# Kernel tuning notes

Measured on AMD Instinct MI355X. Metric: run time of the kernel, lower is better.

## Reference

```python
import jax, jax.numpy as jnp
import numpy as np

B, NV, NRINGS, NDIRS, NF = 4, 50000, 3, 16, 16


def setup_inputs() -> dict:
    key = jax.random.key(0)
    k1, k2, k3, k4 = jax.random.split(key, 4)
    basepoints = jax.random.normal(k1, (B, NV, 3), dtype=jnp.float32)
    local_frames = jax.random.normal(k2, (B, NV, 3, 3), dtype=jnp.float32)
    # expmap: gather_nd indices into basepoints' (batch, vertex) dims
    vidx = jax.random.randint(k3, (B, NV, NRINGS, NDIRS), 0, NV, dtype=jnp.int32)
    bidx = jnp.broadcast_to(jnp.arange(B, dtype=jnp.int32)[:, None, None, None],
                            (B, NV, NRINGS, NDIRS))
    expmap = jnp.stack([bidx, vidx], axis=-1)  # (B, NV, NRINGS, NDIRS, 2)
    kernel = jax.random.normal(k4, (NRINGS, NDIRS, 3, NF), dtype=jnp.float32) * 0.05
    bias = jnp.zeros((NF,), dtype=jnp.float32)
    return {"basepoints": basepoints, "local_frames": local_frames,
            "expmap": expmap, "kernel": kernel, "bias": bias}


def reference(basepoints, local_frames, expmap, kernel, bias):
    b, nv = basepoints.shape[0], basepoints.shape[1]
    nrings, ndirs = expmap.shape[2], expmap.shape[3]
    nf = kernel.shape[-1]
    # gather_nd: neighbor coordinates per (ring, direction)
    y = basepoints[expmap[..., 0], expmap[..., 1]]          # (b, nv, nrings, ndirs, 3)
    # center at basepoint
    y = y - basepoints[:, :, None, None, :]
    # rotate into local frame
    y = jnp.einsum('bvkl,bvrdl->bvrdk', local_frames, y)    # (b, nv, nrings, ndirs, 3)
    # patch conv with ring wraparound (circular padding along direction axis)
    y = y.reshape(b * nv, nrings, ndirs, 3)
    y = jnp.concatenate([y, y[:, :, :-1, :]], axis=2)       # (b*nv, nrings, 2*ndirs-1, 3)
    y = jax.lax.conv_general_dilated(
        y, kernel, window_strides=(1, 1), padding='VALID',
        dimension_numbers=('NHWC', 'HWIO', 'NHWC'))         # (b*nv, 1, ndirs, nf)
    y = y.reshape(b, nv, ndirs, nf) + bias
    return jax.nn.relu(y)
```

## Files before the change

kernel.cpp:

```cpp
#include <hip/hip_runtime.h>

#define NBATCH 4
#define NV     50000
#define NRINGS 3
#define NDIRS  16
#define NF     16
#define VPB    16
#define YLS    148
#define KTS    20

__global__ __launch_bounds__(256, 4)
void input3d_kernel(const float* __restrict__ bp,
                    const float* __restrict__ fr,
                    const int2*  __restrict__ em,
                    const float* __restrict__ kw,
                    const float* __restrict__ bias,
                    float*       __restrict__ out)
{
    __shared__ __align__(16) float kt[NRINGS * 3 * NF * KTS];
    __shared__ __align__(16) float yl[VPB * YLS];
    __shared__ __align__(16) float ost[VPB * NDIRS * NF];

    const int tid = threadIdx.x;
    const int bv0 = blockIdx.x * VPB;

    for (int i = tid; i < NRINGS * NDIRS * 3 * NF; i += 256) {
        int f  = i & 15;
        int c  = (i >> 4) % 3;
        int dd = (i / 48) & 15;
        int r  = i / 768;
        kt[((r * 3 + c) * 16 + f) * KTS + dd] = kw[i];
    }

    #pragma unroll
    for (int k = 0; k < 3; ++k) {
        int p   = tid + k * 256;
        int v   = p / 48;
        int i48 = p - v * 48;
        int bv  = bv0 + v;
        int2 e  = em[bv * 48 + i48];
        int nb  = e.x * NV + e.y;
        float cx = bp[bv * 3 + 0];
        float cy = bp[bv * 3 + 1];
        float cz = bp[bv * 3 + 2];
        float d0 = bp[nb * 3 + 0] - cx;
        float d1 = bp[nb * 3 + 1] - cy;
        float d2 = bp[nb * 3 + 2] - cz;
        const float* F = fr + (size_t)bv * 9;
        #pragma unroll
        for (int c = 0; c < 3; ++c) {
            float yv = F[c * 3 + 0] * d0
                     + F[c * 3 + 1] * d1
                     + F[c * 3 + 2] * d2;
            yl[v * YLS + c * 48 + i48] = yv;
        }
    }
    __syncthreads();

    const int vloc = tid >> 4;
    const int f    = tid & 15;
    float acc[16];
    #pragma unroll
    for (int d = 0; d < 16; ++d) acc[d] = 0.f;

    const float* ylv = &yl[vloc * YLS];
    #pragma unroll 1
    for (int rc = 0; rc < 9; ++rc) {
        int r = rc / 3;
        int c = rc - r * 3;
        float ylr[16];
        const float4* y4 = (const float4*)(ylv + c * 48 + r * 16);
        *(float4*)&ylr[0]  = y4[0];
        *(float4*)&ylr[4]  = y4[1];
        *(float4*)&ylr[8]  = y4[2];
        *(float4*)&ylr[12] = y4[3];
        float kf[16];
        const float4* k4 = (const float4*)&kt[(rc * 16 + f) * KTS];
        *(float4*)&kf[0]  = k4[0];
        *(float4*)&kf[4]  = k4[1];
        *(float4*)&kf[8]  = k4[2];
        *(float4*)&kf[12] = k4[3];
        #pragma unroll
        for (int dd = 0; dd < 16; ++dd) {
            float kv = kf[dd];
            #pragma unroll
            for (int d = 0; d < 16; ++d)
                acc[d] = fmaf(ylr[(d + dd) & 15], kv, acc[d]);
        }
    }

    float bsf = bias[f];
    #pragma unroll
    for (int d = 0; d < 16; ++d) {
        float o = acc[d] + bsf;
        ost[vloc * 256 + d * 16 + f] = o > 0.f ? o : 0.f;
    }
    __syncthreads();

    const float4* s4 = (const float4*)&ost[tid * 16];
    float4* dst = (float4*)(out + (size_t)bv0 * 256 + (size_t)tid * 16);
    dst[0] = s4[0];
    dst[1] = s4[1];
    dst[2] = s4[2];
    dst[3] = s4[3];
}

extern "C" void kernel_launch(void* const* d_in, const int* in_sizes, int n_in,
                              void* d_out, int out_size, void* d_ws, size_t ws_size,
                              hipStream_t stream) {
    const float* bp   = (const float*)d_in[0];
    const float* fr   = (const float*)d_in[1];
    const int2*  em   = (const int2*)d_in[2];
    const float* kw   = (const float*)d_in[3];
    const float* bias = (const float*)d_in[4];
    float* out = (float*)d_out;

    const int total_bv = NBATCH * NV;
    const int grid = total_bv / VPB;
    input3d_kernel<<<grid, 256, 0, stream>>>(bp, fr, em, kw, bias, out);
}
```

Before: 414.0 us.

## Recast circular patch conv as bf16 MFMA GEMM over duplicated ring buffer

Reformulates the per-vertex circular convolution as a 16x144x16 GEMM run on MFMA 16x16x32 bf16 instructions. Rotated neighbor coordinates are stored in bf16 into a doubled, shifted LDS layout so each output direction row reads a contiguous window. Kernel weights are converted to bf16 straight into registers per lane, and outputs are written directly from the accumulators without the LDS staging pass. The aim is to replace about 2300 scalar FMAs per thread with a few matrix ops, at the cost of reduced precision from bf16 inputs and less coalesced output stores.

```diff
diff --git a/kernel.cpp b/kernel.cpp
--- a/kernel.cpp
+++ b/kernel.cpp
@@ -1,108 +1,123 @@
 #include <hip/hip_runtime.h>
+#include <hip/hip_bf16.h>
 
 #define NBATCH 4
 #define NV     50000
-#define NRINGS 3
-#define NDIRS  16
-#define NF     16
 #define VPB    16
-#define YLS    148
-#define KTS    20
+#define VST    304
+
+typedef __attribute__((ext_vector_type(8))) short short8;
+typedef __attribute__((ext_vector_type(4))) float floatx4;
 
 __global__ __launch_bounds__(256, 4)
-void input3d_kernel(const float* __restrict__ bp,
-                    const float* __restrict__ fr,
-                    const int2*  __restrict__ em,
-                    const float* __restrict__ kw,
-                    const float* __restrict__ bias,
-                    float*       __restrict__ out)
+void input3d_mfma(const float* __restrict__ bp,
+                  const float* __restrict__ fr,
+                  const int2*  __restrict__ em,
+                  const float* __restrict__ kw,
+                  const float* __restrict__ bias,
+                  float*       __restrict__ out)
 {
-    __shared__ __align__(16) float kt[NRINGS * 3 * NF * KTS];
-    __shared__ __align__(16) float yl[VPB * YLS];
-    __shared__ __align__(16) float ost[VPB * NDIRS * NF];
+    __shared__ __align__(16) unsigned short yls[VPB * 2 * VST];
 
-    const int tid = threadIdx.x;
-    const int bv0 = blockIdx.x * VPB;
+    const int tid  = threadIdx.x;
+    const int bv0  = blockIdx.x * VPB;
+    const int lane = tid & 63;
+    const int wid  = tid >> 6;
+    const int fcol = lane & 15;
+    const int quad = lane >> 4;
 
-    for (int i = tid; i < NRINGS * NDIRS * 3 * NF; i += 256) {
-        int f  = i & 15;
-        int c  = (i >> 4) % 3;
-        int dd = (i / 48) & 15;
-        int r  = i / 768;
-        kt[((r * 3 + c) * 16 + f) * KTS + dd] = kw[i];
+    for (int i = tid; i < VPB * 51; i += 256) {
+        int v = i / 51;
+        int w = i - v * 51;
+        int off = (w < 25) ? (279 + w) : (VST + 278 + (w - 25));
+        yls[v * 2 * VST + off] = 0;
     }
 
+    union WU { short s[8]; short8 v; };
+    WU wf[5];
     #pragma unroll
-    for (int k = 0; k < 3; ++k) {
-        int p   = tid + k * 256;
+    for (int kc = 0; kc < 5; ++kc) {
+        #pragma unroll
+        for (int j = 0; j < 8; ++j) {
+            int k = kc * 32 + quad * 8 + j;
+            unsigned short b = 0;
+            if (k < 144) {
+                int dd = k / 9;
+                int q  = k - dd * 9;
+                int r  = q / 3;
+                int c  = q - r * 3;
+                __hip_bfloat16 h = __float2bfloat16(kw[((r * 16 + dd) * 3 + c) * 16 + fcol]);
+                __builtin_memcpy(&b, &h, 2);
+            }
+            wf[kc].s[j] = (short)b;
+        }
+    }
+    const float bsf = bias[fcol];
+
+    #pragma unroll
+    for (int t = 0; t < 3; ++t) {
+        int p   = tid + t * 256;
         int v   = p / 48;
         int i48 = p - v * 48;
+        int r   = i48 >> 4;
+        int dir = i48 & 15;
         int bv  = bv0 + v;
         int2 e  = em[bv * 48 + i48];
         int nb  = e.x * NV + e.y;
-        float cx = bp[bv * 3 + 0];
-        float cy = bp[bv * 3 + 1];
-        float cz = bp[bv * 3 + 2];
-        float d0 = bp[nb * 3 + 0] - cx;
-        float d1 = bp[nb * 3 + 1] - cy;
-        float d2 = bp[nb * 3 + 2] - cz;
+        float dx = bp[nb * 3 + 0] - bp[bv * 3 + 0];
+        float dy = bp[nb * 3 + 1] - bp[bv * 3 + 1];
+        float dz = bp[nb * 3 + 2] - bp[bv * 3 + 2];
         const float* F = fr + (size_t)bv * 9;
+        unsigned short* buf = &yls[v * 2 * VST];
         #pragma unroll
         for (int c = 0; c < 3; ++c) {
-            float yv = F[c * 3 + 0] * d0
-                     + F[c * 3 + 1] * d1
-                     + F[c * 3 + 2] * d2;
-            yl[v * YLS + c * 48 + i48] = yv;
+            float yv = F[c * 3 + 0] * dx + F[c * 3 + 1] * dy + F[c * 3 + 2] * dz;
+            __hip_bfloat16 h = __float2bfloat16(yv);
+            unsigned short us;
+            __builtin_memcpy(&us, &h, 2);
+            int q  = r * 3 + c;
+            int e1 = dir * 9 + q;
+            buf[e1] = us;
+            if (e1 > 0) buf[VST + e1 - 1] = us;
+            if (dir < 15) {
+                buf[e1 + 144] = us;
+                buf[VST + e1 + 143] = us;
+            }
         }
     }
     __syncthreads();
 
-    const int vloc = tid >> 4;
-    const int f    = tid & 15;
-    float acc[16];
+    floatx4 acc[4] = {{0.f,0.f,0.f,0.f},{0.f,0.f,0.f,0.f},
+                      {0.f,0.f,0.f,0.f},{0.f,0.f,0.f,0.f}};
+    const unsigned short* abase[4];
     #pragma unroll
-    for (int d = 0; d < 16; ++d) acc[d] = 0.f;
-
-    const float* ylv = &yl[vloc * YLS];
-    #pragma unroll 1
-    for (int rc = 0; rc < 9; ++rc) {
-        int r = rc / 3;
-        int c = rc - r * 3;
-        float ylr[16];
-        const float4* y4 = (const float4*)(ylv + c * 48 + r * 16);
-        *(float4*)&ylr[0]  = y4[0];
-        *(float4*)&ylr[4]  = y4[1];
-        *(float4*)&ylr[8]  = y4[2];
-        *(float4*)&ylr[12] = y4[3];
-        float kf[16];
-        const float4* k4 = (const float4*)&kt[(rc * 16 + f) * KTS];
-        *(float4*)&kf[0]  = k4[0];
-        *(float4*)&kf[4]  = k4[1];
-        *(float4*)&kf[8]  = k4[2];
-        *(float4*)&kf[12] = k4[3];
+    for (int i = 0; i < 4; ++i) {
+        int v = wid * 4 + i;
+        abase[i] = &yls[v * 2 * VST + ((fcol & 1) ? (VST - 1) : 0) + 9 * fcol];
+    }
+    #pragma unroll
+    for (int kc = 0; kc < 5; ++kc) {
+        const int s = kc * 32 + quad * 8;
         #pragma unroll
-        for (int dd = 0; dd < 16; ++dd) {
-            float kv = kf[dd];
-            #pragma unroll
-            for (int d = 0; d < 16; ++d)
-                acc[d] = fmaf(ylr[(d + dd) & 15], kv, acc[d]);
+        for (int i = 0; i < 4; ++i) {
+            const unsigned int* pa = (const unsigned int*)(abase[i] + s);
+            union { unsigned int u[4]; short8 s8; } a;
+            a.u[0] = pa[0]; a.u[1] = pa[1]; a.u[2] = pa[2]; a.u[3] = pa[3];
+            acc[i] = __builtin_amdgcn_mfma_f32_16x16x32_bf16(a.s8, wf[kc].v, acc[i], 0, 0, 0);
         }
     }
 
-    float bsf = bias[f];
     #pragma unroll
-    for (int d = 0; d < 16; ++d) {
-        float o = acc[d] + bsf;
-        ost[vloc * 256 + d * 16 + f] = o > 0.f ? o : 0.f;
+    for (int i = 0; i < 4; ++i) {
+        int vg = bv0 + wid * 4 + i;
+        float* ob = out + (size_t)vg * 256;
+        #pragma unroll
+        for (int rr = 0; rr < 4; ++rr) {
+            float o = acc[i][rr] + bsf;
+            o = o > 0.f ? o : 0.f;
+            ob[(quad * 4 + rr) * 16 + fcol] = o;
+        }
     }
-    __syncthreads();
-
-    const float4* s4 = (const float4*)&ost[tid * 16];
-    float4* dst = (float4*)(out + (size_t)bv0 * 256 + (size_t)tid * 16);
-    dst[0] = s4[0];
-    dst[1] = s4[1];
-    dst[2] = s4[2];
-    dst[3] = s4[3];
 }
 
 extern "C" void kernel_launch(void* const* d_in, const int* in_sizes, int n_in,
@@ -117,5 +132,5 @@
 
     const int total_bv = NBATCH * NV;
     const int grid = total_bv / VPB;
-    input3d_kernel<<<grid, 256, 0, stream>>>(bp, fr, em, kw, bias, out);
+    input3d_mfma<<<grid, 256, 0, stream>>>(bp, fr, em, kw, bias, out);
 }
```

New measurement: 367.4 us. 11.3% less time.
